# Optimization experiments

Measured on AMD Instinct MI355X. Metric: run time of the kernel, lower is better.

## Reference

```python
import jax, jax.numpy as jnp
import numpy as np
import math

EPS = 1e-6
ROPE_BASE = 10000.0

def _rmsnorm(x, w):
    # normalize over last dim (head_dim)
    rms = jax.lax.rsqrt(jnp.mean(x * x, axis=-1, keepdims=True) + EPS)
    return x * rms * w

def _rope_cos_sin(seq_len, head_dim, dtype):
    inv_freq = 1.0 / (ROPE_BASE ** (jnp.arange(0, head_dim, 2, dtype=jnp.float32) / head_dim))
    t = jnp.arange(seq_len, dtype=jnp.float32)
    freqs = jnp.outer(t, inv_freq)            # [S, Dh/2]
    emb = jnp.concatenate([freqs, freqs], -1)  # [S, Dh]
    return jnp.cos(emb).astype(dtype), jnp.sin(emb).astype(dtype)

def _rotate_half(x):
    half = x.shape[-1] // 2
    return jnp.concatenate([-x[..., half:], x[..., :half]], axis=-1)

def setup_inputs() -> dict:
    key = jax.random.key(0)
    ks = jax.random.split(key, 6)
    B, S, E = 1, 2048, 2048
    H, KVH, Dh = 16, 4, 128
    x = jax.random.normal(ks[0], (B, S, E), dtype=jnp.float32)
    mask = jnp.triu(jnp.ones((S, S), dtype=bool), k=1)  # True = masked (causal)
    scale = 0.02
    Wq = jax.random.normal(ks[1], (E, E), dtype=jnp.float32) * scale
    Wk = jax.random.normal(ks[2], (KVH * Dh, E), dtype=jnp.float32) * scale
    Wv = jax.random.normal(ks[3], (KVH * Dh, E), dtype=jnp.float32) * scale
    Wo = jax.random.normal(ks[4], (E, E), dtype=jnp.float32) * scale
    q_norm_w = jnp.ones((Dh,), dtype=jnp.float32)
    k_norm_w = jnp.ones((Dh,), dtype=jnp.float32)
    return {"x": x, "mask": mask, "Wq": Wq, "Wk": Wk, "Wv": Wv, "Wo": Wo,
            "q_norm_w": q_norm_w, "k_norm_w": k_norm_w}

def reference(x, mask, Wq, Wk, Wv, Wo, q_norm_w, k_norm_w):
    B, S, E = x.shape
    H, Dh = 16, E // 16
    KVH = Wk.shape[0] // Dh
    rep = H // KVH
    # QKV projections (torch Linear: x @ W.T)
    q = (x @ Wq.T).reshape(B, S, H, Dh).transpose(0, 2, 1, 3)    # [B,H,S,Dh]
    k = (x @ Wk.T).reshape(B, S, KVH, Dh).transpose(0, 2, 1, 3)  # [B,KVH,S,Dh]
    v = (x @ Wv.T).reshape(B, S, KVH, Dh).transpose(0, 2, 1, 3)
    # QK-RMSNorm
    q = _rmsnorm(q, q_norm_w)
    k = _rmsnorm(k, k_norm_w)
    # RoPE
    cos, sin = _rope_cos_sin(S, Dh, q.dtype)  # [S,Dh]
    q = q * cos + _rotate_half(q) * sin
    k = k * cos + _rotate_half(k) * sin
    # GQA expand kv heads (repeat_interleave on head dim)
    k = jnp.repeat(k, rep, axis=1)  # [B,H,S,Dh]
    v = jnp.repeat(v, rep, axis=1)
    # SDPA (no yarn => scale = 1/sqrt(head_dim))
    scale = 1.0 / math.sqrt(Dh)
    scores = jnp.einsum('bhqd,bhkd->bhqk', q, k) * scale
    scores = jnp.where(mask[None, None, :, :], -jnp.inf, scores)
    attn = jax.nn.softmax(scores, axis=-1)
    attn = jnp.nan_to_num(attn, nan=0.0)
    out = jnp.einsum('bhqk,bhkd->bhqd', attn, v)
    out = out.transpose(0, 2, 1, 3).reshape(B, S, E)
    return out @ Wo.T
```

## Files before the change

kernel.cpp:

```cpp
#include <hip/hip_runtime.h>
#include <hip/hip_bf16.h>
#include <cstdint>
#include <cstddef>

using bf16 = __hip_bfloat16;
typedef __attribute__((ext_vector_type(8))) short short8;
typedef __attribute__((ext_vector_type(4))) float f32x4;
typedef __attribute__((ext_vector_type(4))) unsigned int u32x4;

#define MFMA16(a, b, c) __builtin_amdgcn_mfma_f32_16x16x32_bf16((a), (b), (c), 0, 0, 0)

static constexpr int S = 2048;
static constexpr int E = 2048;
static constexpr int H = 16;
static constexpr int KVH = 4;
static constexpr int Dh = 128;
static constexpr int NQKV = 3072;
static constexpr float ATTN_SCALE = 0.08838834764831845f;
static constexpr float NEG_BIG = -1e30f;

__device__ __forceinline__ short f2bs(float f) {
  __hip_bfloat16 h = __float2bfloat16(f);
  return *reinterpret_cast<short*>(&h);
}

__device__ __forceinline__ unsigned int pack_bf16(float lo, float hi) {
  return ((unsigned int)(unsigned short)f2bs(hi) << 16) |
         (unsigned int)(unsigned short)f2bs(lo);
}

__device__ __forceinline__ void gload_lds16(const void* g, void* l) {
  __builtin_amdgcn_global_load_lds(
      (const __attribute__((address_space(1))) unsigned int*)g,
      (__attribute__((address_space(3))) unsigned int*)l,
      16, 0, 0);
}

__global__ void cvt_bf16(const float* __restrict__ src, bf16* __restrict__ dst, int n) {
  int i = (blockIdx.x * 256 + threadIdx.x) * 8;
  if (i + 8 > n) return;
  const float4* s4 = reinterpret_cast<const float4*>(src + i);
  float4 a = s4[0];
  float4 b = s4[1];
  short8 o;
  o[0] = f2bs(a.x); o[1] = f2bs(a.y); o[2] = f2bs(a.z); o[3] = f2bs(a.w);
  o[4] = f2bs(b.x); o[5] = f2bs(b.y); o[6] = f2bs(b.z); o[7] = f2bs(b.w);
  *reinterpret_cast<short8*>(dst + i) = o;
}

template <bool OUT_F32>
__global__ __launch_bounds__(256, 2) void gemm_nt(const bf16* __restrict__ A,
                                                  const bf16* __restrict__ B,
                                                  void* __restrict__ Cout,
                                                  int M, int N, int K) {
  __shared__ bf16 As[128 * 32];
  __shared__ bf16 Bs[128 * 32];
  const int tid = threadIdx.x;
  const int lane = tid & 63;
  const int wv = tid >> 6;
  const int lr = lane & 15, lq = lane >> 4;
  const int wm = (wv >> 1) * 64, wn = (wv & 1) * 64;

  const int nwgx = M >> 7;
  const int nwg = (M >> 7) * (N >> 7);
  const int id = blockIdx.x + gridDim.x * blockIdx.y;
  const int sid = (id & 7) * (nwg >> 3) + (id >> 3);
  const int bm = (sid % nwgx) * 128, bn = (sid / nwgx) * 128;

  f32x4 acc[4][4] = {};

  for (int k0 = 0; k0 < K; k0 += 32) {
    __syncthreads();
    for (int it = 0; it < 2; ++it) {
      int ci = it * 256 + tid;
      int row = ci >> 2, co = (ci & 3) * 8;
      gload_lds16(A + (size_t)(bm + row) * K + k0 + co, As + (it * 256 + wv * 64) * 8);
      gload_lds16(B + (size_t)(bn + row) * K + k0 + co, Bs + (it * 256 + wv * 64) * 8);
    }
    __syncthreads();

    short8 af[4], bfr[4];
#pragma unroll
    for (int im = 0; im < 4; ++im)
      af[im] = *reinterpret_cast<const short8*>(As + (wm + im * 16 + lr) * 32 + lq * 8);
#pragma unroll
    for (int jn = 0; jn < 4; ++jn)
      bfr[jn] = *reinterpret_cast<const short8*>(Bs + (wn + jn * 16 + lr) * 32 + lq * 8);
#pragma unroll
    for (int im = 0; im < 4; ++im)
#pragma unroll
      for (int jn = 0; jn < 4; ++jn)
        acc[im][jn] = MFMA16(af[im], bfr[jn], acc[im][jn]);
  }

#pragma unroll
  for (int im = 0; im < 4; ++im)
#pragma unroll
    for (int jn = 0; jn < 4; ++jn)
#pragma unroll
      for (int i = 0; i < 4; ++i) {
        int r = bm + wm + im * 16 + lq * 4 + i;
        int c = bn + wn + jn * 16 + lr;
        if (OUT_F32)
          reinterpret_cast<float*>(Cout)[(size_t)r * N + c] = acc[im][jn][i];
        else
          reinterpret_cast<bf16*>(Cout)[(size_t)r * N + c] = __float2bfloat16(acc[im][jn][i]);
      }
}

__global__ __launch_bounds__(256, 2) void gemm_nt64(const bf16* __restrict__ A,
                                                    const bf16* __restrict__ B,
                                                    float* __restrict__ Cout,
                                                    int M, int N, int K) {
  __shared__ bf16 As[128 * 32];
  __shared__ bf16 Bs[64 * 32];
  const int tid = threadIdx.x;
  const int lane = tid & 63;
  const int wv = tid >> 6;
  const int lr = lane & 15, lq = lane >> 4;
  const int wm = (wv >> 1) * 64, wn = (wv & 1) * 32;

  const int nwgx = M >> 7;
  const int nwg = (M >> 7) * (N >> 6);
  const int id = blockIdx.x + gridDim.x * blockIdx.y;
  const int sid = (id & 7) * (nwg >> 3) + (id >> 3);
  const int bm = (sid % nwgx) * 128, bn = (sid / nwgx) * 64;

  f32x4 acc[4][2] = {};

  for (int k0 = 0; k0 < K; k0 += 32) {
    __syncthreads();
#pragma unroll
    for (int it = 0; it < 2; ++it) {
      int ci = it * 256 + tid;
      int row = ci >> 2, co = (ci & 3) * 8;
      gload_lds16(A + (size_t)(bm + row) * K + k0 + co, As + (it * 256 + wv * 64) * 8);
    }
    {
      int ci = tid;
      int row = ci >> 2, co = (ci & 3) * 8;
      gload_lds16(B + (size_t)(bn + row) * K + k0 + co, Bs + (wv * 64) * 8);
    }
    __syncthreads();

    short8 af[4], bfr[2];
#pragma unroll
    for (int im = 0; im < 4; ++im)
      af[im] = *reinterpret_cast<const short8*>(As + (wm + im * 16 + lr) * 32 + lq * 8);
#pragma unroll
    for (int jn = 0; jn < 2; ++jn)
      bfr[jn] = *reinterpret_cast<const short8*>(Bs + (wn + jn * 16 + lr) * 32 + lq * 8);
#pragma unroll
    for (int im = 0; im < 4; ++im)
#pragma unroll
      for (int jn = 0; jn < 2; ++jn)
        acc[im][jn] = MFMA16(af[im], bfr[jn], acc[im][jn]);
  }

#pragma unroll
  for (int im = 0; im < 4; ++im)
#pragma unroll
    for (int jn = 0; jn < 2; ++jn)
#pragma unroll
      for (int i = 0; i < 4; ++i) {
        int r = bm + wm + im * 16 + lq * 4 + i;
        int c = bn + wn + jn * 16 + lr;
        Cout[(size_t)r * N + c] = acc[im][jn][i];
      }
}

__global__ void qk_norm_rope(const bf16* __restrict__ QKV,
                             const float* __restrict__ qw, const float* __restrict__ kw,
                             bf16* __restrict__ Qn, bf16* __restrict__ Kn) {
  const int lane = threadIdx.x & 63;
  const int w = threadIdx.x >> 6;
  const int row = blockIdx.x * 4 + w;
  const int s = row / 20;
  const int hh = row % 20;

  const bf16* src;
  bf16* dst;
  const float* wt;
  float outscale;
  if (hh < 16) {
    src = QKV + (size_t)s * NQKV + hh * Dh;
    dst = Qn + ((size_t)hh * S + s) * Dh;
    wt = qw;
    outscale = ATTN_SCALE;
  } else {
    int kvh = hh - 16;
    src = QKV + (size_t)s * NQKV + 2048 + kvh * Dh;
    dst = Kn + ((size_t)kvh * S + s) * Dh;
    wt = kw;
    outscale = 1.0f;
  }

  float x0 = __bfloat162float(src[lane]);
  float x1 = __bfloat162float(src[lane + 64]);
  float ss = x0 * x0 + x1 * x1;
#pragma unroll
  for (int off = 1; off < 64; off <<= 1) ss += __shfl_xor(ss, off);
  float rms = rsqrtf(ss * (1.0f / 128.0f) + 1e-6f);
  float n0 = x0 * rms * wt[lane];
  float n1 = x1 * rms * wt[lane + 64];

  float inv_freq = exp2f((float)lane * -0.2076205059304601f);
  float ang = (float)s * inv_freq;
  float sn, cs;
  sincosf(ang, &sn, &cs);
  float o0 = (n0 * cs - n1 * sn) * outscale;
  float o1 = (n1 * cs + n0 * sn) * outscale;
  dst[lane] = __float2bfloat16(o0);
  dst[lane + 64] = __float2bfloat16(o1);
}

__global__ void v_transpose(const bf16* __restrict__ QKV, bf16* __restrict__ Vt) {
  __shared__ bf16 t[64][65];
  const int s0 = blockIdx.x * 64;
  const int c0 = blockIdx.y * 64;
  const int kvh = c0 >> 7, d0 = c0 & 127;
#pragma unroll 4
  for (int i = 0; i < 16; ++i) {
    int lin = i * 256 + threadIdx.x;
    int r = lin >> 6, c = lin & 63;
    t[r][c] = QKV[(size_t)(s0 + r) * NQKV + 2560 + c0 + c];
  }
  __syncthreads();
#pragma unroll 4
  for (int i = 0; i < 16; ++i) {
    int lin = i * 256 + threadIdx.x;
    int d = lin >> 6, s = lin & 63;
    Vt[((size_t)kvh * 128 + d0 + d) * S + s0 + s] = t[s][d];
  }
}

__device__ __forceinline__ void chunk_decode(int u, int& qi, int& c, int& nc) {
  if (u < 8)       { qi = u;               c = 0;      nc = 1; }
  else if (u < 24) { int v = u - 8;  qi = 8  + (v >> 1); c = v & 1;  nc = 2; }
  else if (u < 48) { int v = u - 24; qi = 16 + v / 3;    c = v % 3;  nc = 3; }
  else             { int v = u - 48; qi = 24 + (v >> 2); c = v & 3;  nc = 4; }
}

__global__ __launch_bounds__(256, 2) void attn_fwd(const bf16* __restrict__ Qn,
                                                   const bf16* __restrict__ Kn,
                                                   const bf16* __restrict__ Vt,
                                                   bf16* __restrict__ AO,
                                                   bf16* __restrict__ Opart,
                                                   float* __restrict__ ml) {
  __shared__ bf16 Ks[2][64 * 128];
  __shared__ bf16 Vs[2][128 * 64];

  const int tid = threadIdx.x;
  const int lane = tid & 63;
  const int w = tid >> 6;
  const int lr = lane & 15, lq = lane >> 4;

  const int bx = blockIdx.x;
  const int h = bx / 80, u = bx % 80;
  int qi, cch, nc;
  chunk_decode(u, qi, cch, nc);
  const int kvh = h >> 2;
  const int q0 = qi * 64;
  const int t0 = cch * 8;
  const int t1 = min(t0 + 8, qi + 1);

  const bf16* Qbase = Qn + ((size_t)h * S + q0 + w * 16) * Dh;
  const bf16* Kbase = Kn + (size_t)kvh * S * Dh;
  const bf16* Vbase = Vt + (size_t)kvh * Dh * S;

  short8 qf[4];
#pragma unroll
  for (int dd = 0; dd < 4; ++dd)
    qf[dd] = *reinterpret_cast<const short8*>(Qbase + (size_t)lr * Dh + dd * 32 + lq * 8);

  short8 ones;
#pragma unroll
  for (int e = 0; e < 8; ++e) ones[e] = (short)0x3F80;

  float m = NEG_BIG;
  f32x4 lacc = {};
  f32x4 oacc[8] = {};

  auto stageK = [&](int tile, int b) {
    const int kb = tile * 64;
#pragma unroll
    for (int i = 0; i < 4; ++i) {
      int chunk = i * 256 + tid;
      int r = chunk >> 4, c = chunk & 15;
      int cs = c ^ (r & 7);
      gload_lds16(Kbase + (size_t)(kb + r) * Dh + cs * 8,
                  (bf16*)Ks + b * 8192 + (i * 256 + w * 64) * 8);
    }
  };
  auto stageV = [&](int tile, int b) {
    const int kb = tile * 64;
#pragma unroll
    for (int i = 0; i < 4; ++i) {
      int chunk = i * 256 + tid;
      int r = chunk >> 3, c = chunk & 7;
      int cs = c ^ (r & 7);
      gload_lds16(Vbase + (size_t)r * S + kb + cs * 8,
                  (bf16*)Vs + b * 8192 + (i * 256 + w * 64) * 8);
    }
  };

  stageK(t0, 0);
  stageV(t0, 0);
  __syncthreads();
  int buf = 0;

  for (int t = t0; t < t1; ++t) {
    if (t + 1 < t1) { stageK(t + 1, buf ^ 1); stageV(t + 1, buf ^ 1); }

    f32x4 sacc[4] = {};
    __builtin_amdgcn_s_setprio(1);
#pragma unroll
    for (int jn = 0; jn < 4; ++jn) {
      int r = jn * 16 + lr;
      const char* kroww = (const char*)Ks + buf * 16384 + r * 256;
      int rx = r & 7;
#pragma unroll
      for (int dd = 0; dd < 4; ++dd) {
        int cg = (dd * 4 + lq) ^ rx;
        short8 kf = *reinterpret_cast<const short8*>(kroww + cg * 16);
        sacc[jn] = MFMA16(kf, qf[dd], sacc[jn]);
      }
    }
    __builtin_amdgcn_s_setprio(0);

    const bool diag = (t == qi);
    float p[4][4];
    float pm = NEG_BIG;
#pragma unroll
    for (int jn = 0; jn < 4; ++jn)
#pragma unroll
      for (int i = 0; i < 4; ++i) {
        float v = sacc[jn][i];
        if (diag && (jn * 16 + lq * 4 + i > w * 16 + lr)) v = NEG_BIG;
        p[jn][i] = v;
        pm = fmaxf(pm, v);
      }
    pm = fmaxf(pm, __shfl_xor(pm, 16));
    pm = fmaxf(pm, __shfl_xor(pm, 32));

    if (!__all(pm - m <= 8.0f)) {
      float mnew = fmaxf(m, pm);
      float a = __expf(m - mnew);
      m = mnew;
      float aq[4];
#pragma unroll
      for (int i = 0; i < 4; ++i) aq[i] = __shfl(a, lq * 4 + i);
#pragma unroll
      for (int i = 0; i < 4; ++i) {
        lacc[i] *= aq[i];
#pragma unroll
        for (int jd = 0; jd < 8; ++jd) oacc[jd][i] *= aq[i];
      }
    }

    unsigned int wd[4][2];
#pragma unroll
    for (int jn = 0; jn < 4; ++jn)
#pragma unroll
      for (int uu = 0; uu < 2; ++uu) {
        float plo = __expf(p[jn][2 * uu] - m);
        float phi = __expf(p[jn][2 * uu + 1] - m);
        wd[jn][uu] = pack_bf16(plo, phi);
      }

    short8 pa[2];
#pragma unroll
    for (int kk = 0; kk < 2; ++kk) {
      u32x4 w4;
#pragma unroll
      for (int tt = 0; tt < 4; ++tt) {
        int sl = lr + 16 * ((lq & 1) * 2 + (tt >> 1));
        unsigned int s0 = __shfl(wd[kk * 2][tt & 1], sl);
        unsigned int s1 = __shfl(wd[kk * 2 + 1][tt & 1], sl);
        w4[tt] = (lq >> 1) ? s1 : s0;
      }
      pa[kk] = __builtin_bit_cast(short8, w4);
    }

    __builtin_amdgcn_s_setprio(1);
#pragma unroll
    for (int kk = 0; kk < 2; ++kk) {
      lacc = MFMA16(pa[kk], ones, lacc);
#pragma unroll
      for (int jd = 0; jd < 8; ++jd) {
        int r = jd * 16 + lr;
        int cg = (kk * 4 + lq) ^ (r & 7);
        short8 vf = *reinterpret_cast<const short8*>((const char*)Vs + buf * 16384 + r * 128 + cg * 16);
        oacc[jd] = MFMA16(pa[kk], vf, oacc[jd]);
      }
    }
    __builtin_amdgcn_s_setprio(0);

    __syncthreads();
    buf ^= 1;
  }

  if (nc == 1) {
#pragma unroll
    for (int jd = 0; jd < 8; ++jd)
#pragma unroll
      for (int i = 0; i < 4; ++i) {
        float o = oacc[jd][i] / lacc[i];
        AO[(size_t)(q0 + w * 16 + lq * 4 + i) * E + h * Dh + jd * 16 + lr] = __float2bfloat16(o);
      }
  } else {
    const int pidx = h * 80 + u;
    bf16* Op = Opart + (size_t)pidx * 64 * 128;
#pragma unroll
    for (int jd = 0; jd < 8; ++jd)
#pragma unroll
      for (int i = 0; i < 4; ++i)
        Op[(w * 16 + lq * 4 + i) * 128 + jd * 16 + lr] = __float2bfloat16(oacc[jd][i]);
    if (lq == 0)
      ml[(size_t)pidx * 128 + (w * 16 + lr) * 2] = m;
    if (lr == 0) {
#pragma unroll
      for (int i = 0; i < 4; ++i)
        ml[(size_t)pidx * 128 + (w * 16 + lq * 4 + i) * 2 + 1] = lacc[i];
    }
  }
}

__global__ __launch_bounds__(256) void attn_combine(const bf16* __restrict__ Opart,
                                                    const float* __restrict__ ml,
                                                    bf16* __restrict__ AO) {
  const int qi = 8 + blockIdx.x;
  const int h = blockIdx.y;
  const int nc = qi / 8 + 1;
  const int off = (qi < 16) ? 8 + (qi - 8) * 2
                : (qi < 24) ? 24 + (qi - 16) * 3
                            : 48 + (qi - 24) * 4;
  const int base = h * 80 + off;
  const int row = threadIdx.x >> 2;
  const int d0 = (threadIdx.x & 3) * 32;

  float mc[4], lc[4];
  float M = -INFINITY;
  for (int c = 0; c < nc; ++c) {
    mc[c] = ml[(size_t)(base + c) * 128 + row * 2];
    lc[c] = ml[(size_t)(base + c) * 128 + row * 2 + 1];
    M = fmaxf(M, mc[c]);
  }
  float L = 0.0f;
  float acc[32];
#pragma unroll
  for (int j = 0; j < 32; ++j) acc[j] = 0.0f;
  for (int c = 0; c < nc; ++c) {
    float wgt = __expf(mc[c] - M);
    L += wgt * lc[c];
    const short8* op = reinterpret_cast<const short8*>(
        Opart + (size_t)(base + c) * 8192 + row * 128 + d0);
#pragma unroll
    for (int j4 = 0; j4 < 4; ++j4) {
      short8 vv = op[j4];
#pragma unroll
      for (int e = 0; e < 8; ++e) {
        short sv = vv[e];
        acc[j4 * 8 + e] += wgt * __bfloat162float(*reinterpret_cast<bf16*>(&sv));
      }
    }
  }
  float inv = 1.0f / L;
  bf16* ao = AO + (size_t)(qi * 64 + row) * E + h * Dh + d0;
  short8 outv[4];
#pragma unroll
  for (int j4 = 0; j4 < 4; ++j4) {
#pragma unroll
    for (int e = 0; e < 8; ++e) outv[j4][e] = f2bs(acc[j4 * 8 + e] * inv);
    reinterpret_cast<short8*>(ao)[j4] = outv[j4];
  }
}

extern "C" void kernel_launch(void* const* d_in, const int* in_sizes, int n_in,
                              void* d_out, int out_size, void* d_ws, size_t ws_size,
                              hipStream_t stream) {
  const float* x  = (const float*)d_in[0];
  const float* Wq = (const float*)d_in[2];
  const float* Wk = (const float*)d_in[3];
  const float* Wv = (const float*)d_in[4];
  const float* Wo = (const float*)d_in[5];
  const float* qw = (const float*)d_in[6];
  const float* kw = (const float*)d_in[7];

  char* ws = (char*)d_ws;
  bf16* xb   = (bf16*)(ws + (0ull << 20));
  bf16* Wcat = (bf16*)(ws + (8ull << 20));
  bf16* Wob  = (bf16*)(ws + (20ull << 20));
  bf16* QKV  = (bf16*)(ws + (28ull << 20));
  bf16* Qn   = (bf16*)(ws + (40ull << 20));
  bf16* Kn   = (bf16*)(ws + (48ull << 20));
  bf16* Vt   = (bf16*)(ws + (50ull << 20));
  bf16* AO   = (bf16*)(ws + (52ull << 20));
  bf16* Opart = (bf16*)(ws + (0ull << 20));
  float* ml   = (float*)(ws + (28ull << 20));

  cvt_bf16<<<2048, 256, 0, stream>>>(x, xb, E * S);
  cvt_bf16<<<2048, 256, 0, stream>>>(Wq, Wcat, E * E);
  cvt_bf16<<<512, 256, 0, stream>>>(Wk, Wcat + 2048 * 2048, 512 * E);
  cvt_bf16<<<512, 256, 0, stream>>>(Wv, Wcat + 2560 * 2048, 512 * E);
  cvt_bf16<<<2048, 256, 0, stream>>>(Wo, Wob, E * E);

  gemm_nt<false><<<dim3(S / 128, NQKV / 128), 256, 0, stream>>>(xb, Wcat, QKV, S, NQKV, E);

  qk_norm_rope<<<(S * 20) / 4, 256, 0, stream>>>(QKV, qw, kw, Qn, Kn);
  v_transpose<<<dim3(S / 64, 512 / 64), 256, 0, stream>>>(QKV, Vt);

  attn_fwd<<<16 * 80, 256, 0, stream>>>(Qn, Kn, Vt, AO, Opart, ml);
  attn_combine<<<dim3(24, 16), 256, 0, stream>>>(Opart, ml, AO);

  gemm_nt64<<<dim3(S / 128, E / 64), 256, 0, stream>>>(AO, Wob, (float*)d_out, S, E, E);
}
```

Measured before the change: 174.8 us.

## Merge conversion kernels and stage V tiles through registers with single LDS buffer

Replaces the five float-to-bf16 conversion launches with one kernel that dispatches on a flat index range, cutting launch overhead. In attention, V tiles are now loaded into registers during compute and written into a single LDS buffer after the barrier, instead of double-buffered async global-to-LDS loads. This halves V LDS usage, which could raise occupancy, but adds register pressure, an extra barrier per tile, and exposed LDS write latency.

```diff
diff --git a/kernel.cpp b/kernel.cpp
--- a/kernel.cpp
+++ b/kernel.cpp
@@ -36,16 +36,28 @@
       16, 0, 0);
 }
 
-__global__ void cvt_bf16(const float* __restrict__ src, bf16* __restrict__ dst, int n) {
-  int i = (blockIdx.x * 256 + threadIdx.x) * 8;
-  if (i + 8 > n) return;
-  const float4* s4 = reinterpret_cast<const float4*>(src + i);
+__global__ void cvt_all(const float* __restrict__ x,  const float* __restrict__ wq,
+                        const float* __restrict__ wk, const float* __restrict__ wv,
+                        const float* __restrict__ wo,
+                        bf16* __restrict__ xb, bf16* __restrict__ wcat,
+                        bf16* __restrict__ wob) {
+  const long M1 = 4l << 20, M2 = 8l << 20, M3 = 9l << 20, M4 = 10l << 20, M5 = 14l << 20;
+  long i = ((long)blockIdx.x * 256 + threadIdx.x) * 8;
+  if (i >= M5) return;
+  const float* src;
+  bf16* dst;
+  if (i < M1)      { src = x  + i;        dst = xb + i; }
+  else if (i < M2) { src = wq + (i - M1); dst = wcat + (i - M1); }
+  else if (i < M3) { src = wk + (i - M2); dst = wcat + 2048l * 2048 + (i - M2); }
+  else if (i < M4) { src = wv + (i - M3); dst = wcat + 2560l * 2048 + (i - M3); }
+  else             { src = wo + (i - M4); dst = wob + (i - M4); }
+  const float4* s4 = reinterpret_cast<const float4*>(src);
   float4 a = s4[0];
   float4 b = s4[1];
   short8 o;
   o[0] = f2bs(a.x); o[1] = f2bs(a.y); o[2] = f2bs(a.z); o[3] = f2bs(a.w);
   o[4] = f2bs(b.x); o[5] = f2bs(b.y); o[6] = f2bs(b.z); o[7] = f2bs(b.w);
-  *reinterpret_cast<short8*>(dst + i) = o;
+  *reinterpret_cast<short8*>(dst) = o;
 }
 
 template <bool OUT_F32>
@@ -248,7 +260,7 @@
                                                    bf16* __restrict__ Opart,
                                                    float* __restrict__ ml) {
   __shared__ bf16 Ks[2][64 * 128];
-  __shared__ bf16 Vs[2][128 * 64];
+  __shared__ bf16 Vs[128 * 64];
 
   const int tid = threadIdx.x;
   const int lane = tid & 63;
@@ -280,6 +292,7 @@
   float m = NEG_BIG;
   f32x4 lacc = {};
   f32x4 oacc[8] = {};
+  float4 vreg[4];
 
   auto stageK = [&](int tile, int b) {
     const int kb = tile * 64;
@@ -292,25 +305,34 @@
                   (bf16*)Ks + b * 8192 + (i * 256 + w * 64) * 8);
     }
   };
-  auto stageV = [&](int tile, int b) {
+  auto loadV = [&](int tile) {
     const int kb = tile * 64;
 #pragma unroll
-    for (int i = 0; i < 4; ++i) {
-      int chunk = i * 256 + tid;
+    for (int j = 0; j < 4; ++j) {
+      int chunk = j * 256 + tid;
+      int r = chunk >> 3, c = chunk & 7;
+      vreg[j] = *reinterpret_cast<const float4*>(Vbase + (size_t)r * S + kb + c * 8);
+    }
+  };
+  auto writeV = [&]() {
+#pragma unroll
+    for (int j = 0; j < 4; ++j) {
+      int chunk = j * 256 + tid;
       int r = chunk >> 3, c = chunk & 7;
       int cs = c ^ (r & 7);
-      gload_lds16(Vbase + (size_t)r * S + kb + cs * 8,
-                  (bf16*)Vs + b * 8192 + (i * 256 + w * 64) * 8);
+      *reinterpret_cast<float4*>((char*)Vs + r * 128 + cs * 16) = vreg[j];
     }
   };
 
   stageK(t0, 0);
-  stageV(t0, 0);
+  loadV(t0);
   __syncthreads();
+  writeV();
   int buf = 0;
 
   for (int t = t0; t < t1; ++t) {
-    if (t + 1 < t1) { stageK(t + 1, buf ^ 1); stageV(t + 1, buf ^ 1); }
+    __syncthreads();
+    if (t + 1 < t1) { stageK(t + 1, buf ^ 1); loadV(t + 1); }
 
     f32x4 sacc[4] = {};
     __builtin_amdgcn_s_setprio(1);
@@ -390,13 +412,14 @@
       for (int jd = 0; jd < 8; ++jd) {
         int r = jd * 16 + lr;
         int cg = (kk * 4 + lq) ^ (r & 7);
-        short8 vf = *reinterpret_cast<const short8*>((const char*)Vs + buf * 16384 + r * 128 + cg * 16);
+        short8 vf = *reinterpret_cast<const short8*>((const char*)Vs + r * 128 + cg * 16);
         oacc[jd] = MFMA16(pa[kk], vf, oacc[jd]);
       }
     }
     __builtin_amdgcn_s_setprio(0);
 
     __syncthreads();
+    if (t + 1 < t1) writeV();
     buf ^= 1;
   }
 
@@ -499,11 +522,7 @@
   bf16* Opart = (bf16*)(ws + (0ull << 20));
   float* ml   = (float*)(ws + (28ull << 20));
 
-  cvt_bf16<<<2048, 256, 0, stream>>>(x, xb, E * S);
-  cvt_bf16<<<2048, 256, 0, stream>>>(Wq, Wcat, E * E);
-  cvt_bf16<<<512, 256, 0, stream>>>(Wk, Wcat + 2048 * 2048, 512 * E);
-  cvt_bf16<<<512, 256, 0, stream>>>(Wv, Wcat + 2560 * 2048, 512 * E);
-  cvt_bf16<<<2048, 256, 0, stream>>>(Wo, Wob, E * E);
+  cvt_all<<<7168, 256, 0, stream>>>(x, Wq, Wk, Wv, Wo, xb, Wcat, Wob);
 
   gemm_nt<false><<<dim3(S / 128, NQKV / 128), 256, 0, stream>>>(xb, Wcat, QKV, S, NQKV, E);
 
```

Result: slower. 183.5 us (+5.0%).
